# Kernel optimization log

Measured on AMD Instinct MI355X. Metric: run time of the kernel, lower is better.

## Reference

```python
import jax, jax.numpy as jnp
import numpy as np

N = 100_000       # nodes
E = 1_600_000     # edges (avg degree 16)
IN_DIM = 256
OUT_DIM = 64
NEG_SLOPE = 0.01  # F.leaky_relu default


def setup_inputs() -> dict:
    key = jax.random.key(0)
    k1, k2, k3, k4, k5 = jax.random.split(key, 5)
    h = jax.random.normal(k1, (N, IN_DIM), jnp.float32)
    fc_w = jax.random.normal(k2, (IN_DIM, OUT_DIM), jnp.float32) / np.sqrt(IN_DIM)
    attn_w = jax.random.normal(k3, (2 * OUT_DIM,), jnp.float32) / np.sqrt(2 * OUT_DIM)
    src = jax.random.randint(k4, (E,), 0, N, jnp.int32)
    dst = jax.random.randint(k5, (E,), 0, N, jnp.int32)
    return {"h": h, "fc_w": fc_w, "attn_w": attn_w, "src": src, "dst": dst}


def reference(h, fc_w, attn_w, src, dst):
    # z = fc(h)
    z = h @ fc_w                                    # [N, D]
    # attn_fc(cat(z_src, z_dst)) == z_src @ a_l + z_dst @ a_r
    s_src = z @ attn_w[:OUT_DIM]                    # [N]
    s_dst = z @ attn_w[OUT_DIM:]                    # [N]
    e = jax.nn.leaky_relu(s_src[src] + s_dst[dst], NEG_SLOPE)  # [E]
    # per-destination segment softmax (stable)
    e_max = jax.ops.segment_max(e, dst, num_segments=N)        # [N]
    e_max = jnp.where(jnp.isfinite(e_max), e_max, 0.0)         # nodes w/o in-edges
    ex = jnp.exp(e - e_max[dst])                               # [E]
    denom = jax.ops.segment_sum(ex, dst, num_segments=N)       # [N]
    alpha = ex / jnp.maximum(denom[dst], 1e-9)                 # [E]
    # weighted scatter-sum of source features
    h_out = jax.ops.segment_sum(alpha[:, None] * z[src], dst, num_segments=N)  # [N, D]
    return h_out
```

## Files before the change

### kernel.cpp

```cpp
#include <hip/hip_runtime.h>
#include <hip/hip_bf16.h>
#include <math.h>

#define IN_DIM 256
#define OUT_DIM 64
#define NEG_SLOPE 0.01f
#define NBSHIFT 7
#define BNODES 128
#define BCAP 2560
#define A_CHUNK 4096

typedef __attribute__((ext_vector_type(8))) short short8;
typedef __attribute__((ext_vector_type(4))) float f32x4;

__device__ __forceinline__ unsigned short f2bf_rne(float f) {
    unsigned u = __builtin_bit_cast(unsigned, f);
    u += 0x7FFF + ((u >> 16) & 1);
    return (unsigned short)(u >> 16);
}
__device__ __forceinline__ float bflo(unsigned v) {
    return __builtin_bit_cast(float, v << 16);
}
__device__ __forceinline__ float bfhi(unsigned v) {
    return __builtin_bit_cast(float, v & 0xFFFF0000u);
}
__device__ __forceinline__ unsigned cvtpk_bf16(float lo, float hi) {
    unsigned r;
    asm("v_cvt_pk_bf16_f32 %0, %1, %2" : "=v"(r) : "v"(lo), "v"(hi));
    return r;
}

__global__ __launch_bounds__(256) void k_prep(
    const float* __restrict__ fcw, unsigned short* __restrict__ bhi,
    int* __restrict__ gcnt, int NB)
{
    int t = blockIdx.x * 256 + threadIdx.x;
    if (t < NB) gcnt[t] = 0;
    if (t >= 2048) return;
    int lane = t & 63;
    int nt = (t >> 6) & 3;
    int step = t >> 8;
    int kbase = step * 32 + (lane >> 4) * 8;
    int col = nt * 16 + (lane & 15);
#pragma unroll
    for (int i = 0; i < 8; ++i)
        bhi[t * 8 + i] = f2bf_rne(fcw[(size_t)(kbase + i) * OUT_DIM + col]);
}

__global__ __launch_bounds__(256, 4) void k_gemm(
    const float* __restrict__ h, const unsigned short* __restrict__ bhi,
    const float* __restrict__ attnw, unsigned short* __restrict__ zb,
    float* __restrict__ ssrc, float* __restrict__ sdst, int nrows)
{
    __shared__ short8 Bs[2048];
    const int tid = threadIdx.x;
    const int lane = tid & 63;
    const int wid = tid >> 6;
    const int rowbase = blockIdx.x * 64 + wid * 16;
    const int arow = rowbase + (lane & 15);
    const size_t abase = (size_t)min(arow, nrows - 1) * IN_DIM + (lane >> 4) * 8;

    float4 a[16];
#pragma unroll
    for (int s = 0; s < 8; ++s) {
        a[2 * s]     = *(const float4*)&h[abase + s * 32];
        a[2 * s + 1] = *(const float4*)&h[abase + s * 32 + 4];
    }
    asm volatile("" ::: "memory");

    short8 breg[8];
#pragma unroll
    for (int c = 0; c < 8; ++c)
        breg[c] = *(const short8*)&bhi[(c * 256 + tid) * 8];
#pragma unroll
    for (int c = 0; c < 8; ++c)
        Bs[c * 256 + tid] = breg[c];
    __syncthreads();

    short8 abf[8];
#pragma unroll
    for (int step = 0; step < 8; ++step) {
        uint4 pk;
        pk.x = cvtpk_bf16(a[2 * step].x,     a[2 * step].y);
        pk.y = cvtpk_bf16(a[2 * step].z,     a[2 * step].w);
        pk.z = cvtpk_bf16(a[2 * step + 1].x, a[2 * step + 1].y);
        pk.w = cvtpk_bf16(a[2 * step + 1].z, a[2 * step + 1].w);
        abf[step] = __builtin_bit_cast(short8, pk);
    }

    f32x4 acc[4] = {};
#pragma unroll
    for (int step = 0; step < 8; ++step) {
#pragma unroll
        for (int nt = 0; nt < 4; ++nt) {
            short8 bh = Bs[(step * 4 + nt) * 64 + lane];
            acc[nt] = __builtin_amdgcn_mfma_f32_16x16x32_bf16(
                abf[step], bh, acc[nt], 0, 0, 0);
        }
    }
    __syncthreads();

    unsigned short* zst = (unsigned short*)Bs;
    const int col = lane & 15;
    float aw1[4], aw2[4];
#pragma unroll
    for (int nt = 0; nt < 4; ++nt) {
        aw1[nt] = attnw[nt * 16 + col];
        aw2[nt] = attnw[OUT_DIM + nt * 16 + col];
    }
#pragma unroll
    for (int r = 0; r < 4; ++r) {
        int lrow = wid * 16 + (lane >> 4) * 4 + r;
        int grow = blockIdx.x * 64 + lrow;
        float ss = 0.f, sd = 0.f;
#pragma unroll
        for (int nt = 0; nt < 4; ++nt) {
            float v = acc[nt][r];
            ss = fmaf(v, aw1[nt], ss);
            sd = fmaf(v, aw2[nt], sd);
            zst[lrow * 72 + nt * 16 + col] = f2bf_rne(v);
        }
#pragma unroll
        for (int m = 8; m; m >>= 1) {
            ss += __shfl_xor(ss, m);
            sd += __shfl_xor(sd, m);
        }
        if (col == 0 && grow < nrows) { ssrc[grow] = ss; sdst[grow] = sd; }
    }
    __syncthreads();

    {
        int lrow = tid >> 2;
        int c0 = (tid & 3) * 16;
        int grow = blockIdx.x * 64 + lrow;
        if (grow < nrows) {
            uint4 v0 = *(const uint4*)&zst[lrow * 72 + c0];
            uint4 v1 = *(const uint4*)&zst[lrow * 72 + c0 + 8];
            *(uint4*)&zb[(size_t)grow * OUT_DIM + c0] = v0;
            *(uint4*)&zb[(size_t)grow * OUT_DIM + c0 + 8] = v1;
        }
    }
}

__global__ __launch_bounds__(256) void k_bin(
    const int* __restrict__ src, const int* __restrict__ dst,
    int* __restrict__ gcnt, int* __restrict__ gbuf, int E, int NB)
{
    __shared__ int cnt[1024];
    __shared__ int base[1024];
    int t = threadIdx.x;
    for (int i = t; i < NB; i += 256) cnt[i] = 0;
    __syncthreads();
    int ebase = blockIdx.x * A_CHUNK;
    int bkt[16], pkd[16];
#pragma unroll
    for (int i = 0; i < 16; ++i) {
        int e = ebase + t + i * 256;
        bkt[i] = -1;
        if (e < E) {
            int d = dst[e];
            int b = ((unsigned)d) >> NBSHIFT;
            bkt[i] = b;
            pkd[i] = ((d & (BNODES - 1)) << 24) | src[e];
            atomicAdd(&cnt[b], 1);
        }
    }
    __syncthreads();
    for (int i = t; i < NB; i += 256) {
        int c = cnt[i];
        base[i] = c ? (i * BCAP + atomicAdd(&gcnt[i], c)) : 0;
    }
    __syncthreads();
#pragma unroll
    for (int i = 0; i < 16; ++i) {
        if (bkt[i] >= 0) {
            int r = atomicAdd(&base[bkt[i]], 1);
            gbuf[r] = pkd[i];
        }
    }
}

__global__ __launch_bounds__(256) void k_aggr(
    const int* __restrict__ gcnt, const int* __restrict__ gbuf,
    const float* __restrict__ ssrc, const float* __restrict__ sdst,
    const unsigned short* __restrict__ zb, float* __restrict__ out, int N)
{
    __shared__ float2 pairs[BCAP];
    __shared__ int   ldeg[BNODES];
    __shared__ int   cur[BNODES];
    __shared__ float lsd[BNODES];
    __shared__ int2  se[BNODES];
    const int t = threadIdx.x;
    const int b = blockIdx.x;
    const int eb = b * BCAP;
    const int cnt = min(gcnt[b], BCAP);

    if (t < BNODES) {
        int node0 = (b << NBSHIFT) + t;
        ldeg[t] = 0;
        lsd[t] = (node0 < N) ? sdst[node0] : 0.f;
    }
    __syncthreads();
    for (int i = t; i < cnt; i += 256)
        atomicAdd(&ldeg[((unsigned)gbuf[eb + i]) >> 24], 1);
    __syncthreads();
    int own = (t < BNODES) ? ldeg[t] : 0;
    for (int o = 1; o < BNODES; o <<= 1) {
        int x = 0;
        if (t < BNODES && t >= o) x = ldeg[t - o];
        __syncthreads();
        if (t < BNODES && t >= o) ldeg[t] += x;
        __syncthreads();
    }
    if (t < BNODES) {
        int excl = ldeg[t] - own;
        cur[t] = excl;
        se[t] = make_int2(excl, excl + own);
    }
    __syncthreads();

    for (int cb = 0; cb < cnt; cb += 4096) {
        const int nloc = min(4096, cnt - cb);
        int p[16]; float w[16];
#pragma unroll
        for (int k = 0; k < 16; ++k) {
            int i = t + k * 256;
            if (i < nloc) {
                p[k] = gbuf[eb + cb + i];
                float x = ssrc[p[k] & 0xFFFFFF] + lsd[((unsigned)p[k]) >> 24];
                x = (x > 0.f) ? x : NEG_SLOPE * x;
                w[k] = __expf(x);
            }
        }
#pragma unroll
        for (int k = 0; k < 16; ++k) {
            int i = t + k * 256;
            if (i < nloc) {
                int r = atomicAdd(&cur[((unsigned)p[k]) >> 24], 1);
                pairs[r] = make_float2(
                    w[k], __builtin_bit_cast(float, (p[k] & 0xFFFFFF) << 7));
            }
        }
    }
    __syncthreads();

    const int g = t >> 4;
    const int li8 = (t & 15) * 8;
#pragma unroll
    for (int j = 0; j < BNODES / 16; ++j) {
        const int ln = g * (BNODES / 16) + j;
        const int node = (b << NBSHIFT) + ln;
        if (node >= N) continue;
        const int2 s = se[ln];
        float denom = 0.f, a0 = 0.f, a1 = 0.f, a2 = 0.f, a3 = 0.f;
        for (int i0 = s.x; i0 < s.y; i0 += 8) {
            float w8[8]; int off8[8]; uint2 v8[8];
#pragma unroll
            for (int k = 0; k < 8; ++k) {
                int idx = i0 + k;
                bool ok = idx < s.y;
                float2 pw = pairs[ok ? idx : s.x];
                w8[k] = ok ? pw.x : 0.f;
                off8[k] = __builtin_bit_cast(int, pw.y) + li8;
            }
#pragma unroll
            for (int k = 0; k < 8; ++k)
                v8[k] = *(const uint2*)((const char*)zb + off8[k]);
#pragma unroll
            for (int k = 0; k < 8; ++k) {
                a0 = fmaf(w8[k], bflo(v8[k].x), a0);
                a1 = fmaf(w8[k], bfhi(v8[k].x), a1);
                a2 = fmaf(w8[k], bflo(v8[k].y), a2);
                a3 = fmaf(w8[k], bfhi(v8[k].y), a3);
                denom += w8[k];
            }
        }
        const float inv = 1.f / fmaxf(denom, 1e-9f);
        *(float4*)&out[(size_t)node * OUT_DIM + (t & 15) * 4] =
            make_float4(a0 * inv, a1 * inv, a2 * inv, a3 * inv);
    }
}

extern "C" void kernel_launch(void* const* d_in, const int* in_sizes, int n_in,
                              void* d_out, int out_size, void* d_ws, size_t ws_size,
                              hipStream_t stream)
{
    const float* h     = (const float*)d_in[0];
    const float* fcw   = (const float*)d_in[1];
    const float* attnw = (const float*)d_in[2];
    const int*   src   = (const int*)d_in[3];
    const int*   dst   = (const int*)d_in[4];
    const int N = in_sizes[0] / IN_DIM;
    const int E = in_sizes[3];
    float* out = (float*)d_out;

    const int NB = (N + BNODES - 1) >> NBSHIFT;
    const int NWGA = (E + A_CHUNK - 1) / A_CHUNK;

    char* ws = (char*)d_ws;
    size_t off = 0;
    auto carve = [&](size_t bytes) -> void* {
        void* p = ws + off;
        off = (off + bytes + 255) & ~(size_t)255;
        return p;
    };
    unsigned short* zb = (unsigned short*)carve((size_t)N * OUT_DIM * 2);
    float* ssrc     = (float*)carve((size_t)N * 4);
    float* sdst     = (float*)carve((size_t)N * 4);
    int*   gbuf     = (int*)carve((size_t)NB * BCAP * 4);
    unsigned short* bhi = (unsigned short*)carve(2048 * 8 * 2);
    int* gcnt  = (int*)carve((size_t)NB * 4);

    k_prep<<<8, 256, 0, stream>>>(fcw, bhi, gcnt, NB);
    k_gemm<<<(N + 63) / 64, 256, 0, stream>>>(h, bhi, attnw, zb, ssrc, sdst, N);
    k_bin<<<NWGA, 256, 0, stream>>>(src, dst, gcnt, gbuf, E, NB);
    k_aggr<<<NB, 256, 0, stream>>>(gcnt, gbuf, ssrc, sdst, zb, out, N);
}
```

Measured before the change: 100.3 us.

## Fuse edge binning with fp32-to-bf16 conversion of h, GEMM reads bf16

Merges the edge-binning kernel with a new pass that converts h from fp32 to bf16 into a workspace buffer, sharing one launch. The GEMM then loads bf16 A-tiles directly instead of converting in registers. This overlaps binning with a bandwidth-bound conversion and shrinks GEMM register pressure and load volume. In exchange it adds a full extra write and read of a bf16 copy of h, which raises total memory traffic.

```diff
diff --git a/kernel.cpp b/kernel.cpp
--- a/kernel.cpp
+++ b/kernel.cpp
@@ -47,8 +47,69 @@
         bhi[t * 8 + i] = f2bf_rne(fcw[(size_t)(kbase + i) * OUT_DIM + col]);
 }
 
+__global__ __launch_bounds__(256) void k_binconv(
+    const int* __restrict__ src, const int* __restrict__ dst,
+    int* __restrict__ gcnt, int* __restrict__ gbuf, int E, int NB,
+    const float* __restrict__ h, unsigned short* __restrict__ hb,
+    int N, int nbin)
+{
+    __shared__ int cnt[1024];
+    __shared__ int base[1024];
+    const int bid = blockIdx.x;
+    const int t = threadIdx.x;
+
+    if (bid < nbin) {
+        for (int i = t; i < NB; i += 256) cnt[i] = 0;
+        __syncthreads();
+        int ebase = bid * A_CHUNK;
+        int bkt[16], pkd[16];
+#pragma unroll
+        for (int i = 0; i < 16; ++i) {
+            int e = ebase + t + i * 256;
+            bkt[i] = -1;
+            if (e < E) {
+                int d = dst[e];
+                int b = ((unsigned)d) >> NBSHIFT;
+                bkt[i] = b;
+                pkd[i] = ((d & (BNODES - 1)) << 24) | src[e];
+                atomicAdd(&cnt[b], 1);
+            }
+        }
+        __syncthreads();
+        for (int i = t; i < NB; i += 256) {
+            int c = cnt[i];
+            base[i] = c ? (i * BCAP + atomicAdd(&gcnt[i], c)) : 0;
+        }
+        __syncthreads();
+#pragma unroll
+        for (int i = 0; i < 16; ++i) {
+            if (bkt[i] >= 0) {
+                int r = atomicAdd(&base[bkt[i]], 1);
+                gbuf[r] = pkd[i];
+            }
+        }
+    }
+
+    {
+        const int rb = bid * 128;
+        const int rows = min(128, N - rb);
+        if (rows > 0) {
+            const int nf4 = rows * (IN_DIM / 4);
+            const float4* hp = (const float4*)&h[(size_t)rb * IN_DIM];
+            uint2* op = (uint2*)&hb[(size_t)rb * IN_DIM];
+            for (int i = t; i < nf4; i += 256) {
+                float4 v = hp[i];
+                uint2 o;
+                o.x = cvtpk_bf16(v.x, v.y);
+                o.y = cvtpk_bf16(v.z, v.w);
+                op[i] = o;
+            }
+        }
+    }
+}
+
 __global__ __launch_bounds__(256, 4) void k_gemm(
-    const float* __restrict__ h, const unsigned short* __restrict__ bhi,
+    const unsigned short* __restrict__ hb, const unsigned short* __restrict__ bhi,
     const float* __restrict__ attnw, unsigned short* __restrict__ zb,
     float* __restrict__ ssrc, float* __restrict__ sdst, int nrows)
 {
@@ -60,12 +121,10 @@
     const int arow = rowbase + (lane & 15);
     const size_t abase = (size_t)min(arow, nrows - 1) * IN_DIM + (lane >> 4) * 8;
 
-    float4 a[16];
-#pragma unroll
-    for (int s = 0; s < 8; ++s) {
-        a[2 * s]     = *(const float4*)&h[abase + s * 32];
-        a[2 * s + 1] = *(const float4*)&h[abase + s * 32 + 4];
-    }
+    short8 abf[8];
+#pragma unroll
+    for (int s = 0; s < 8; ++s)
+        abf[s] = *(const short8*)&hb[abase + s * 32];
     asm volatile("" ::: "memory");
 
     short8 breg[8];
@@ -76,17 +135,6 @@
     for (int c = 0; c < 8; ++c)
         Bs[c * 256 + tid] = breg[c];
     __syncthreads();
-
-    short8 abf[8];
-#pragma unroll
-    for (int step = 0; step < 8; ++step) {
-        uint4 pk;
-        pk.x = cvtpk_bf16(a[2 * step].x,     a[2 * step].y);
-        pk.y = cvtpk_bf16(a[2 * step].z,     a[2 * step].w);
-        pk.z = cvtpk_bf16(a[2 * step + 1].x, a[2 * step + 1].y);
-        pk.w = cvtpk_bf16(a[2 * step + 1].z, a[2 * step + 1].w);
-        abf[step] = __builtin_bit_cast(short8, pk);
-    }
 
     f32x4 acc[4] = {};
 #pragma unroll
@@ -142,44 +190,6 @@
     }
 }
 
-__global__ __launch_bounds__(256) void k_bin(
-    const int* __restrict__ src, const int* __restrict__ dst,
-    int* __restrict__ gcnt, int* __restrict__ gbuf, int E, int NB)
-{
-    __shared__ int cnt[1024];
-    __shared__ int base[1024];
-    int t = threadIdx.x;
-    for (int i = t; i < NB; i += 256) cnt[i] = 0;
-    __syncthreads();
-    int ebase = blockIdx.x * A_CHUNK;
-    int bkt[16], pkd[16];
-#pragma unroll
-    for (int i = 0; i < 16; ++i) {
-        int e = ebase + t + i * 256;
-        bkt[i] = -1;
-        if (e < E) {
-            int d = dst[e];
-            int b = ((unsigned)d) >> NBSHIFT;
-            bkt[i] = b;
-            pkd[i] = ((d & (BNODES - 1)) << 24) | src[e];
-            atomicAdd(&cnt[b], 1);
-        }
-    }
-    __syncthreads();
-    for (int i = t; i < NB; i += 256) {
-        int c = cnt[i];
-        base[i] = c ? (i * BCAP + atomicAdd(&gcnt[i], c)) : 0;
-    }
-    __syncthreads();
-#pragma unroll
-    for (int i = 0; i < 16; ++i) {
-        if (bkt[i] >= 0) {
-            int r = atomicAdd(&base[bkt[i]], 1);
-            gbuf[r] = pkd[i];
-        }
-    }
-}
-
 __global__ __launch_bounds__(256) void k_aggr(
     const int* __restrict__ gcnt, const int* __restrict__ gbuf,
     const float* __restrict__ ssrc, const float* __restrict__ sdst,
@@ -295,7 +305,8 @@
     float* out = (float*)d_out;
 
     const int NB = (N + BNODES - 1) >> NBSHIFT;
-    const int NWGA = (E + A_CHUNK - 1) / A_CHUNK;
+    const int nbin = (E + A_CHUNK - 1) / A_CHUNK;
+    const int nconv = (N + 127) / 128;
 
     char* ws = (char*)d_ws;
     size_t off = 0;
@@ -305,6 +316,7 @@
         return p;
     };
     unsigned short* zb = (unsigned short*)carve((size_t)N * OUT_DIM * 2);
+    unsigned short* hb = (unsigned short*)carve((size_t)N * IN_DIM * 2);
     float* ssrc     = (float*)carve((size_t)N * 4);
     float* sdst     = (float*)carve((size_t)N * 4);
     int*   gbuf     = (int*)carve((size_t)NB * BCAP * 4);
@@ -312,7 +324,8 @@
     int* gcnt  = (int*)carve((size_t)NB * 4);
 
     k_prep<<<8, 256, 0, stream>>>(fcw, bhi, gcnt, NB);
-    k_gemm<<<(N + 63) / 64, 256, 0, stream>>>(h, bhi, attnw, zb, ssrc, sdst, N);
-    k_bin<<<NWGA, 256, 0, stream>>>(src, dst, gcnt, gbuf, E, NB);
+    k_binconv<<<max(nconv, nbin), 256, 0, stream>>>(
+        src, dst, gcnt, gbuf, E, NB, h, hb, N, nbin);
+    k_gemm<<<(N + 63) / 64, 256, 0, stream>>>(hb, bhi, attnw, zb, ssrc, sdst, N);
     k_aggr<<<NB, 256, 0, stream>>>(gcnt, gbuf, ssrc, sdst, zb, out, N);
 }
```

Measured after the change: 111.7 us. +11.3%, slower.
